# Kernel optimization log

Measured on AMD Instinct MI355X. Metric: run time of the kernel, lower is better.

Reference implementation:

```python
import jax, jax.numpy as jnp
import numpy as np

B, T, I, H = 32768, 512, 2, 16  # batch, seq_len, input_size, hidden_size


def setup_inputs() -> dict:
    key = jax.random.key(0)
    ks = jax.random.split(key, 9)
    sc_i = 1.0 / np.sqrt(H)  # torch LSTM/Linear init scale ~ U(-1/sqrt(H), 1/sqrt(H)); use normal*scale
    return {
        "x": jax.random.normal(ks[0], (B, T, I), jnp.float32),
        "W_ih": jax.random.normal(ks[1], (4 * H, I), jnp.float32) * sc_i,
        "W_hh": jax.random.normal(ks[2], (4 * H, H), jnp.float32) * sc_i,
        "b_ih": jax.random.normal(ks[3], (4 * H,), jnp.float32) * sc_i,
        "b_hh": jax.random.normal(ks[4], (4 * H,), jnp.float32) * sc_i,
        "W1": jax.random.normal(ks[5], (H, H), jnp.float32) * sc_i,
        "b1": jax.random.normal(ks[6], (H,), jnp.float32) * sc_i,
        "W2": jax.random.normal(ks[7], (I, H), jnp.float32) * sc_i,
        "b2": jax.random.normal(ks[8], (I,), jnp.float32) * sc_i,
    }


def reference(x, W_ih, W_hh, b_ih, b_hh, W1, b1, W2, b2):
    # x: [B, T, I]. torch forward permutes to (T, B, I) and runs seq-first LSTM.
    # Precompute input projections for all timesteps (one big GEMM): [B, T, 4H]
    x_proj = jnp.einsum('bti,gi->btg', x, W_ih) + b_ih + b_hh
    Whh_T = W_hh.T  # [H, 4H]

    def step(carry, xt):
        h, c = carry                      # [B, H] each
        gates = xt + h @ Whh_T            # [B, 4H]
        i, f, g, o = jnp.split(gates, 4, axis=-1)  # torch gate order: i, f, g, o
        i = jax.nn.sigmoid(i)
        f = jax.nn.sigmoid(f)
        g = jnp.tanh(g)
        o = jax.nn.sigmoid(o)
        c = f * c + i * g
        h = o * jnp.tanh(c)
        return (h, c), None

    bsz = x.shape[0]
    h0 = jnp.zeros((bsz, W_hh.shape[1]), x.dtype)
    c0 = jnp.zeros_like(h0)
    (h_last, _), _ = jax.lax.scan(step, (h0, c0), jnp.swapaxes(x_proj, 0, 1))
    # MLP head on last hidden state: Linear -> tanh -> Linear
    y = jnp.tanh(h_last @ W1.T + b1) @ W2.T + b2  # [B, I]
    return y
```

## Files before the change

kernel.cpp:

```cpp
#include <hip/hip_runtime.h>


#define T_STEPS 512
#define LOG2E 1.44269504088896340736f

typedef __bf16 bf16x8 __attribute__((ext_vector_type(8)));
typedef float  f32x4  __attribute__((ext_vector_type(4)));
typedef float  f32x2  __attribute__((ext_vector_type(2)));
typedef unsigned int u32x4 __attribute__((ext_vector_type(4)));

union frag_u { u32x4 u; bf16x8 v; };

#if __has_builtin(__builtin_amdgcn_exp2f)
__device__ __forceinline__ float fexp2(float x) { return __builtin_amdgcn_exp2f(x); }
#else
__device__ __forceinline__ float fexp2(float x) { return exp2f(x); }
#endif
#if __has_builtin(__builtin_amdgcn_rcpf)
__device__ __forceinline__ float frcp(float x) { return __builtin_amdgcn_rcpf(x); }
#else
__device__ __forceinline__ float frcp(float x) { return 1.0f / x; }
#endif

__device__ __forceinline__ unsigned dup_hi(float h) {
    unsigned hb = __float_as_uint(h);
#if __has_builtin(__builtin_amdgcn_perm)
    return __builtin_amdgcn_perm(hb, hb, 0x03020302u);
#else
    return (hb >> 16) | (hb & 0xFFFF0000u);
#endif
}
__device__ __forceinline__ unsigned lo_with_x(float res, unsigned xq) {
#if __has_builtin(__builtin_amdgcn_perm)
    return __builtin_amdgcn_perm(xq, __float_as_uint(res), 0x07060302u);
#else
    return (__float_as_uint(res) >> 16) | (xq & 0xFFFF0000u);
#endif
}
__device__ __forceinline__ unsigned pack_hilo(float h) {
    unsigned hb = __float_as_uint(h);
    float    res = h - __uint_as_float(hb & 0xFFFF0000u);
#if __has_builtin(__builtin_amdgcn_perm)
    return __builtin_amdgcn_perm(__float_as_uint(res), hb, 0x07060302u);
#else
    return (hb >> 16) | (__float_as_uint(res) & 0xFFFF0000u);
#endif
}
__device__ __forceinline__ unsigned bfhi(float v) {
    return __float_as_uint(v) & 0xFFFF0000u;
}
__device__ __forceinline__ unsigned make_xq(float nx0, float nx1, int q) {
    const float xs = (q & 2) ? nx1 : nx0;
    const unsigned h16 = bfhi(xs);
    const unsigned l16 = bfhi(xs - __uint_as_float(h16));
    return (q & 1) ? l16 : h16;
}

__device__ __forceinline__ void lstm_step_dual(
    const frag_u BhI[2], const frag_u BlI[2],
    frag_u BhO[2], frag_u BlO[2],
    float cst[2][4],
    const frag_u A1[4], const frag_u A2[4], const f32x4 biasf[4],
    unsigned xqA, unsigned xqB)
{
    f32x4 acc[2][4];
    #pragma unroll
    for (int g = 0; g < 2; ++g)
        #pragma unroll
        for (int t = 0; t < 4; ++t)
            acc[g][t] = __builtin_amdgcn_mfma_f32_16x16x32_bf16(A1[t].v, BhI[g].v, biasf[t], 0, 0, 0);
    #pragma unroll
    for (int g = 0; g < 2; ++g)
        #pragma unroll
        for (int t = 0; t < 4; ++t)
            acc[g][t] = __builtin_amdgcn_mfma_f32_16x16x32_bf16(A2[t].v, BlI[g].v, acc[g][t], 0, 0, 0);

    f32x2 eIF[2][4], eGO[2][4];
    #pragma unroll
    for (int g = 0; g < 2; ++g)
        #pragma unroll
        for (int t = 0; t < 4; ++t) {
            eIF[g][t].x = fexp2(acc[g][t][0]);
            eIF[g][t].y = fexp2(acc[g][t][1]);
            eGO[g][t].x = fexp2(acc[g][t][2]);
            eGO[g][t].y = fexp2(acc[g][t][3]);
        }

    float Gm[2][4];
    #pragma unroll
    for (int g = 0; g < 2; ++g)
        #pragma unroll
        for (int t = 0; t < 4; ++t)
            Gm[g][t] = fmaf(2.0f * LOG2E, eGO[g][t].x, -2.0f * LOG2E);

    f32x2 pA[2][4], pB[2][4];
    #pragma unroll
    for (int g = 0; g < 2; ++g)
        #pragma unroll
        for (int t = 0; t < 4; ++t) {
            pA[g][t] = eIF[g][t] + 1.0f;
            pB[g][t] = eGO[g][t] + 1.0f;
        }

    f32x2 PP[2][4];
    #pragma unroll
    for (int g = 0; g < 2; ++g)
        #pragma unroll
        for (int t = 0; t < 4; ++t)
            PP[g][t] = pA[g][t] * pB[g][t];

    float d[2][4], tso[2][4], tsf[2][4], gmp[2][4];
    #pragma unroll
    for (int g = 0; g < 2; ++g)
        #pragma unroll
        for (int t = 0; t < 4; ++t) {
            d[g][t]   = PP[g][t].x * PP[g][t].y;
            tso[g][t] = PP[g][t].x * pA[g][t].y;
            tsf[g][t] = PP[g][t].x * pB[g][t].y;
            gmp[g][t] = Gm[g][t]   * PP[g][t].y;
        }

    float R[2][4];
    #pragma unroll
    for (int g = 0; g < 2; ++g)
        #pragma unroll
        for (int t = 0; t < 4; ++t)
            R[g][t] = frcp(d[g][t]);

    float csn[2][4];
    #pragma unroll
    for (int g = 0; g < 2; ++g)
        #pragma unroll
        for (int t = 0; t < 4; ++t) {
            csn[g][t] = fmaf(tsf[g][t], cst[g][t], gmp[g][t]) * R[g][t];
            cst[g][t] = csn[g][t];
        }

    float C2[2][4];
    #pragma unroll
    for (int g = 0; g < 2; ++g)
        #pragma unroll
        for (int t = 0; t < 4; ++t)
            C2[g][t] = fexp2(csn[g][t]);

    float Rd[2][4];
    #pragma unroll
    for (int g = 0; g < 2; ++g)
        #pragma unroll
        for (int t = 0; t < 4; ++t)
            Rd[g][t] = frcp(C2[g][t] + 1.0f);

    #pragma unroll
    for (int g = 0; g < 2; ++g)
        #pragma unroll
        for (int t = 0; t < 4; ++t) {
            const float tc = fmaf(-2.0f, Rd[g][t], 1.0f);
            const float hn = (tso[g][t] * R[g][t]) * tc;
            const unsigned hb = __float_as_uint(hn);
            BhO[g].u[t] = dup_hi(hn);
            const float resf = hn - __uint_as_float(hb & 0xFFFF0000u);
            BlO[g].u[t] = lo_with_x(resf, g ? xqB : xqA);
        }
}

__global__ __launch_bounds__(256, 1)
void lstm_mfma_kernel(const float* __restrict__ x,
                      const float* __restrict__ W_ih,
                      const float* __restrict__ W_hh,
                      const float* __restrict__ b_ih,
                      const float* __restrict__ b_hh,
                      const float* __restrict__ W1,
                      const float* __restrict__ b1,
                      const float* __restrict__ W2,
                      const float* __restrict__ b2,
                      float* __restrict__ out)
{
    __shared__ float hsm[2][4][16][16];

    const int tid  = threadIdx.x;
    const int wv   = tid >> 6;
    const int lane = tid & 63;
    const int e    = lane & 15;
    const int q    = lane >> 4;
    const int m    = lane & 15;

    const float gsc[4] = { -LOG2E, -LOG2E, 2.0f * LOG2E, -LOG2E };

    frag_u A1[4], A2[4];
    f32x4  biasf[4];
    #pragma unroll
    for (int t = 0; t < 4; ++t) {
        const int   g  = m & 3;
        const int   Rr = g * 16 + 4 * t + (m >> 2);
        const float sc = gsc[g];

        const float xw0 = W_ih[Rr * 2 + 0] * sc;
        const float xw1 = W_ih[Rr * 2 + 1] * sc;
        const unsigned x0h = bfhi(xw0);
        const unsigned x0l = bfhi(xw0 - __uint_as_float(x0h));
        const unsigned x1h = bfhi(xw1);
        const unsigned x1l = bfhi(xw1 - __uint_as_float(x1h));
        const unsigned cw0 = (q < 2) ? x0h : x1h;
        const unsigned cw1 = (q < 2) ? x0l : x1l;

        #pragma unroll
        for (int w = 0; w < 4; ++w) {
            const float whh = W_hh[Rr * 16 + 4 * w + q] * sc;
            A1[t].u[w] = pack_hilo(whh);
            A2[t].u[w] = __float_as_uint(whh) >> 16;
        }
        A2[t].u[0] |= cw0;
        A2[t].u[1] |= cw1;

        #pragma unroll
        for (int j = 0; j < 4; ++j) {
            const int Rb = j * 16 + 4 * t + q;
            biasf[t][j] = (b_ih[Rb] + b_hh[Rb]) * gsc[j];
        }
    }

    const int gelemA = blockIdx.x * 128 + wv * 32 + e;
    const int gelemB = gelemA + 16;
    const float4* xpA = (const float4*)(x + (size_t)gelemA * (T_STEPS * 2));
    const float4* xpB = (const float4*)(x + (size_t)gelemB * (T_STEPS * 2));

    frag_u BhP[2], BlP[2], BhQ[2], BlQ[2];
    float  cst[2][4];
    #pragma unroll
    for (int g = 0; g < 2; ++g)
        #pragma unroll
        for (int t = 0; t < 4; ++t) cst[g][t] = 0.0f;

    float4 xvA = xpA[0];
    float4 xvB = xpB[0];

    {
        const unsigned xA0 = make_xq(xvA.x, xvA.y, q);
        const unsigned xB0 = make_xq(xvB.x, xvB.y, q);
        #pragma unroll
        for (int w = 0; w < 4; ++w) {
            BhP[0].u[w] = 0u; BlP[0].u[w] = xA0;
            BhP[1].u[w] = 0u; BlP[1].u[w] = xB0;
        }
    }

    for (int t2 = 0; t2 < T_STEPS / 2; ++t2) {
        const float4 xnA = xpA[(t2 + 1) & (T_STEPS / 2 - 1)];
        const float4 xnB = xpB[(t2 + 1) & (T_STEPS / 2 - 1)];

        const unsigned xq1A = make_xq(xvA.z, xvA.w, q);
        const unsigned xq1B = make_xq(xvB.z, xvB.w, q);
        const unsigned xq2A = make_xq(xnA.x, xnA.y, q);
        const unsigned xq2B = make_xq(xnB.x, xnB.y, q);

        lstm_step_dual(BhP, BlP, BhQ, BlQ, cst, A1, A2, biasf, xq1A, xq1B);
        lstm_step_dual(BhQ, BlQ, BhP, BlP, cst, A1, A2, biasf, xq2A, xq2B);

        xvA = xnA; xvB = xnB;
    }

    #pragma unroll
    for (int g = 0; g < 2; ++g) {
        #pragma unroll
        for (int r = 0; r < 4; ++r) {
            const float hval = __uint_as_float(BhP[g].u[r] << 16) +
                               __uint_as_float(BlP[g].u[r] << 16);
            hsm[g][wv][e][4 * r + q] = hval;
        }

        float hv[16];
        #pragma unroll
        for (int j = 0; j < 4; ++j) {
            const float4 t4 = *(const float4*)&hsm[g][wv][e][4 * j];
            hv[4 * j + 0] = t4.x; hv[4 * j + 1] = t4.y;
            hv[4 * j + 2] = t4.z; hv[4 * j + 3] = t4.w;
        }

        float z[4];
        #pragma unroll
        for (int r = 0; r < 4; ++r) {
            const int mm = 4 * q + r;
            float a = b1[mm];
            #pragma unroll
            for (int j = 0; j < 16; ++j) a = fmaf(W1[mm * 16 + j], hv[j], a);
            const float E = fexp2(a * (2.0f * LOG2E));
            z[r] = fmaf(-2.0f, frcp(1.0f + E), 1.0f);
        }
        #pragma unroll
        for (int r = 0; r < 4; ++r) hsm[g][wv][e][4 * q + r] = z[r];

        if (q < 2) {
            float a = b2[q];
            #pragma unroll
            for (int j = 0; j < 16; ++j) a = fmaf(W2[q * 16 + j], hsm[g][wv][e][j], a);
            const int gelem = g ? gelemB : gelemA;
            out[(size_t)gelem * 2 + q] = a;
        }
    }
}

extern "C" void kernel_launch(void* const* d_in, const int* in_sizes, int n_in,
                              void* d_out, int out_size, void* d_ws, size_t ws_size,
                              hipStream_t stream) {
    const float* x    = (const float*)d_in[0];
    const float* W_ih = (const float*)d_in[1];
    const float* W_hh = (const float*)d_in[2];
    const float* b_ih = (const float*)d_in[3];
    const float* b_hh = (const float*)d_in[4];
    const float* W1   = (const float*)d_in[5];
    const float* b1   = (const float*)d_in[6];
    const float* W2   = (const float*)d_in[7];
    const float* b2   = (const float*)d_in[8];
    float* out = (float*)d_out;

    lstm_mfma_kernel<<<dim3(256), dim3(256), 0, stream>>>(
        x, W_ih, W_hh, b_ih, b_hh, W1, b1, W2, b2, out);
}
```

Measured before the change: 498.1 us.

## Replace exp2-based gate activations with rational tanh approximations

```diff
diff --git a/kernel.cpp b/kernel.cpp
--- a/kernel.cpp
+++ b/kernel.cpp
@@ -63,6 +63,10 @@
     const frag_u A1[4], const frag_u A2[4], const f32x4 biasf[4],
     unsigned xqA, unsigned xqB)
 {
+    const f32x2 KN1 = {42.0f, 21.0f};
+    const f32x2 KN2 = {2520.0f, 1260.0f};
+    const f32x2 KN3 = {20790.0f, 10395.0f};
+
     f32x4 acc[2][4];
     #pragma unroll
     for (int g = 0; g < 2; ++g)
@@ -75,90 +79,95 @@
         for (int t = 0; t < 4; ++t)
             acc[g][t] = __builtin_amdgcn_mfma_f32_16x16x32_bf16(A2[t].v, BlI[g].v, acc[g][t], 0, 0, 0);
 
-    f32x2 eIF[2][4], eGO[2][4];
-    #pragma unroll
-    for (int g = 0; g < 2; ++g)
-        #pragma unroll
-        for (int t = 0; t < 4; ++t) {
-            eIF[g][t].x = fexp2(acc[g][t][0]);
-            eIF[g][t].y = fexp2(acc[g][t][1]);
-            eGO[g][t].x = fexp2(acc[g][t][2]);
-            eGO[g][t].y = fexp2(acc[g][t][3]);
-        }
-
-    float Gm[2][4];
+    f32x2 a[2][4], b[2][4], ua[2][4], ub[2][4];
+    #pragma unroll
+    for (int g = 0; g < 2; ++g)
+        #pragma unroll
+        for (int t = 0; t < 4; ++t) {
+            a[g][t].x = acc[g][t][0]; a[g][t].y = acc[g][t][1];
+            b[g][t].x = acc[g][t][2]; b[g][t].y = acc[g][t][3];
+            ua[g][t] = a[g][t] * a[g][t];
+            ub[g][t] = b[g][t] * b[g][t];
+        }
+
+    f32x2 numa[2][4], numb[2][4];
+    #pragma unroll
+    for (int g = 0; g < 2; ++g)
+        #pragma unroll
+        for (int t = 0; t < 4; ++t) {
+            f32x2 na = ua[g][t] * 21.0f + 1260.0f;
+            f32x2 nb = ub[g][t] * KN1 + KN2;
+            na = ua[g][t] * na + 10395.0f;
+            nb = ub[g][t] * nb + KN3;
+            numa[g][t] = a[g][t] * na;
+            numb[g][t] = b[g][t] * nb;
+        }
+
+    f32x2 da[2][4], db[2][4];
+    #pragma unroll
+    for (int g = 0; g < 2; ++g)
+        #pragma unroll
+        for (int t = 0; t < 4; ++t) {
+            f32x2 d1 = ua[g][t] + 210.0f;
+            f32x2 d2 = ub[g][t] + 210.0f;
+            d1 = ua[g][t] * d1 + 4725.0f;
+            d2 = ub[g][t] * d2 + 4725.0f;
+            da[g][t] = ua[g][t] * d1 + 10395.0f;
+            db[g][t] = ub[g][t] * d2 + 10395.0f;
+        }
+
+    f32x2 Sa[2][4], Sb[2][4];
+    #pragma unroll
+    for (int g = 0; g < 2; ++g)
+        #pragma unroll
+        for (int t = 0; t < 4; ++t) {
+            Sa[g][t] = da[g][t] + numa[g][t];
+            Sb[g][t] = db[g][t] + numb[g][t];
+        }
+
+    float rp[2][4], num[2][4];
+    #pragma unroll
+    for (int g = 0; g < 2; ++g)
+        #pragma unroll
+        for (int t = 0; t < 4; ++t) {
+            const float A_ = da[g][t].x * db[g][t].x;
+            const float t1 = cst[g][t] * Sa[g][t].y;
+            const float t2 = (Sa[g][t].x * numb[g][t].x) * da[g][t].y;
+            num[g][t] = fmaf(t1, A_, t2);
+            const float P  = A_ * da[g][t].y;
+            rp[g][t] = frcp(P + P);
+        }
+
+    float numc[2][4], dc2[2][4];
+    #pragma unroll
+    for (int g = 0; g < 2; ++g)
+        #pragma unroll
+        for (int t = 0; t < 4; ++t) {
+            const float sn = num[g][t] * rp[g][t];
+            cst[g][t] = sn;
+            const float yc = fminf(fmaxf(sn, -12.0f), 12.0f);
+            const float w  = yc * yc;
+            float nc = fmaf(w, 0.65625f, 157.5f);  nc = fmaf(w, nc, 5197.5f);
+            numc[g][t] = yc * nc;
+            float dc = fmaf(w, 0.015625f, 13.125f); dc = fmaf(w, dc, 1181.25f);
+            dc2[g][t] = fmaf(w, dc, 10395.0f);
+        }
+
+    float rc[2][4];
     #pragma unroll
     for (int g = 0; g < 2; ++g)
         #pragma unroll
         for (int t = 0; t < 4; ++t)
-            Gm[g][t] = fmaf(2.0f * LOG2E, eGO[g][t].x, -2.0f * LOG2E);
-
-    f32x2 pA[2][4], pB[2][4];
-    #pragma unroll
-    for (int g = 0; g < 2; ++g)
-        #pragma unroll
-        for (int t = 0; t < 4; ++t) {
-            pA[g][t] = eIF[g][t] + 1.0f;
-            pB[g][t] = eGO[g][t] + 1.0f;
-        }
-
-    f32x2 PP[2][4];
-    #pragma unroll
-    for (int g = 0; g < 2; ++g)
-        #pragma unroll
-        for (int t = 0; t < 4; ++t)
-            PP[g][t] = pA[g][t] * pB[g][t];
-
-    float d[2][4], tso[2][4], tsf[2][4], gmp[2][4];
-    #pragma unroll
-    for (int g = 0; g < 2; ++g)
-        #pragma unroll
-        for (int t = 0; t < 4; ++t) {
-            d[g][t]   = PP[g][t].x * PP[g][t].y;
-            tso[g][t] = PP[g][t].x * pA[g][t].y;
-            tsf[g][t] = PP[g][t].x * pB[g][t].y;
-            gmp[g][t] = Gm[g][t]   * PP[g][t].y;
-        }
-
-    float R[2][4];
-    #pragma unroll
-    for (int g = 0; g < 2; ++g)
-        #pragma unroll
-        for (int t = 0; t < 4; ++t)
-            R[g][t] = frcp(d[g][t]);
-
-    float csn[2][4];
-    #pragma unroll
-    for (int g = 0; g < 2; ++g)
-        #pragma unroll
-        for (int t = 0; t < 4; ++t) {
-            csn[g][t] = fmaf(tsf[g][t], cst[g][t], gmp[g][t]) * R[g][t];
-            cst[g][t] = csn[g][t];
-        }
-
-    float C2[2][4];
-    #pragma unroll
-    for (int g = 0; g < 2; ++g)
-        #pragma unroll
-        for (int t = 0; t < 4; ++t)
-            C2[g][t] = fexp2(csn[g][t]);
-
-    float Rd[2][4];
-    #pragma unroll
-    for (int g = 0; g < 2; ++g)
-        #pragma unroll
-        for (int t = 0; t < 4; ++t)
-            Rd[g][t] = frcp(C2[g][t] + 1.0f);
-
-    #pragma unroll
-    for (int g = 0; g < 2; ++g)
-        #pragma unroll
-        for (int t = 0; t < 4; ++t) {
-            const float tc = fmaf(-2.0f, Rd[g][t], 1.0f);
-            const float hn = (tso[g][t] * R[g][t]) * tc;
-            const unsigned hb = __float_as_uint(hn);
-            BhO[g].u[t] = dup_hi(hn);
-            const float resf = hn - __uint_as_float(hb & 0xFFFF0000u);
+            rc[g][t] = frcp(db[g][t].y * dc2[g][t]);
+
+    #pragma unroll
+    for (int g = 0; g < 2; ++g)
+        #pragma unroll
+        for (int t = 0; t < 4; ++t) {
+            const float h2 = Sb[g][t].y * (numc[g][t] * rc[g][t]);
+            const unsigned hb = __float_as_uint(h2);
+            BhO[g].u[t] = dup_hi(h2);
+            const float resf = h2 - __uint_as_float(hb & 0xFFFF0000u);
             BlO[g].u[t] = lo_with_x(resf, g ? xqB : xqA);
         }
 }
@@ -184,7 +193,8 @@
     const int q    = lane >> 4;
     const int m    = lane & 15;
 
-    const float gsc[4] = { -LOG2E, -LOG2E, 2.0f * LOG2E, -LOG2E };
+    const float gsc[4]  = { 0.5f, 0.5f, 1.0f, 0.5f };
+    const float gscW[4] = { 0.25f, 0.25f, 0.5f, 0.25f };
 
     frag_u A1[4], A2[4];
     f32x4  biasf[4];
@@ -192,7 +202,8 @@
     for (int t = 0; t < 4; ++t) {
         const int   g  = m & 3;
         const int   Rr = g * 16 + 4 * t + (m >> 2);
-        const float sc = gsc[g];
+        const float sc  = gsc[g];
+        const float scW = gscW[g];
 
         const float xw0 = W_ih[Rr * 2 + 0] * sc;
         const float xw1 = W_ih[Rr * 2 + 1] * sc;
@@ -205,7 +216,7 @@
 
         #pragma unroll
         for (int w = 0; w < 4; ++w) {
-            const float whh = W_hh[Rr * 16 + 4 * w + q] * sc;
+            const float whh = W_hh[Rr * 16 + 4 * w + q] * scW;
             A1[t].u[w] = pack_hilo(whh);
             A2[t].u[w] = __float_as_uint(whh) >> 16;
         }
@@ -263,8 +274,8 @@
     for (int g = 0; g < 2; ++g) {
         #pragma unroll
         for (int r = 0; r < 4; ++r) {
-            const float hval = __uint_as_float(BhP[g].u[r] << 16) +
-                               __uint_as_float(BlP[g].u[r] << 16);
+            const float hval = 0.5f * (__uint_as_float(BhP[g].u[r] << 16) +
+                                       __uint_as_float(BlP[g].u[r] << 16));
             hsm[g][wv][e][4 * r + q] = hval;
         }
 
@@ -280,21 +291,21 @@
         #pragma unroll
         for (int r = 0; r < 4; ++r) {
             const int mm = 4 * q + r;
-            float a = b1[mm];
+            float aa = b1[mm];
             #pragma unroll
-            for (int j = 0; j < 16; ++j) a = fmaf(W1[mm * 16 + j], hv[j], a);
-            const float E = fexp2(a * (2.0f * LOG2E));
+            for (int j = 0; j < 16; ++j) aa = fmaf(W1[mm * 16 + j], hv[j], aa);
+            const float E = fexp2(aa * (2.0f * LOG2E));
             z[r] = fmaf(-2.0f, frcp(1.0f + E), 1.0f);
         }
         #pragma unroll
         for (int r = 0; r < 4; ++r) hsm[g][wv][e][4 * q + r] = z[r];
 
         if (q < 2) {
-            float a = b2[q];
+            float aa = b2[q];
             #pragma unroll
-            for (int j = 0; j < 16; ++j) a = fmaf(W2[q * 16 + j], hsm[g][wv][e][j], a);
+            for (int j = 0; j < 16; ++j) aa = fmaf(W2[q * 16 + j], hsm[g][wv][e][j], aa);
             const int gelem = g ? gelemB : gelemA;
-            out[(size_t)gelem * 2 + q] = a;
+            out[(size_t)gelem * 2 + q] = aa;
         }
     }
 }
```

Result: slower. 598.5 us (+20.2%).
